# Optimization experiments

Hardware: AMD Instinct MI355X
Metric: run time of the kernel (lower is better)

Reference implementation:

```python
import jax, jax.numpy as jnp
import numpy as np


def setup_inputs() -> dict:
    key = jax.random.key(0)
    B, T, I, H = 64, 512, 1024, 1024
    ks = jax.random.split(key, 9)
    scale_x = 1.0 / np.sqrt(I)
    scale_h = 1.0 / np.sqrt(H)
    inp = {"x": jax.random.normal(ks[0], (B, T, I), jnp.float32)}
    names = [("wxi", "whi"), ("wxf", "whf"), ("wxg", "whg"), ("wxo", "who")]
    for g, (nx, nh) in enumerate(names):
        inp[nx] = jax.random.normal(ks[1 + 2 * g], (I, H), jnp.float32) * scale_x
        inp[nh] = jax.random.normal(ks[2 + 2 * g], (H, H), jnp.float32) * scale_h
    for b in ["bxi", "bhi", "bxf", "bhf", "bxg", "bhg", "bxo", "bho"]:
        inp[b] = jnp.zeros((H,), jnp.float32)
    return inp


def reference(x, wxi, bxi, whi, bhi, wxf, bxf, whf, bhf,
              wxg, bxg, whg, bhg, wxo, bxo, who, bho):
    B, T, I = x.shape
    H = whi.shape[0]
    # Precompute all input projections in one big GEMM: (B,T,4H)
    wx = jnp.concatenate([wxi, wxf, wxg, wxo], axis=1)            # (I,4H)
    bx = jnp.concatenate([bxi + bhi, bxf + bhf, bxg + bhg, bxo + bho])  # fold both biases
    xproj = jnp.einsum('bti,ih->bth', x, wx) + bx                 # (B,T,4H)
    wh = jnp.concatenate([whi, whf, whg, who], axis=1)            # (H,4H)

    def step(carry, xp_t):
        h, c = carry                                              # (B,H) each
        gates = xp_t + h @ wh                                     # (B,4H)
        i, f, g, o = jnp.split(gates, 4, axis=-1)
        i = jax.nn.sigmoid(i)
        f = jax.nn.sigmoid(f)
        g = jnp.tanh(g)
        o = jax.nn.sigmoid(o)
        c = f * c + i * g
        h = o * jnp.tanh(c)
        return (h, c), None

    h0 = jnp.zeros((B, H), x.dtype)
    c0 = jnp.zeros((B, H), x.dtype)
    (h_t, c_t), _ = jax.lax.scan(step, (h0, c0), jnp.swapaxes(xproj, 0, 1))
    return (h_t, c_t)
```

## Files before the change

kernel.cpp:

```cpp
#include <hip/hip_runtime.h>

typedef short bf16x8 __attribute__((ext_vector_type(8)));
typedef float f32x4 __attribute__((ext_vector_type(4)));
typedef unsigned long long u64x2 __attribute__((ext_vector_type(2)));

__device__ __forceinline__ unsigned short f2bf(float f) {
  unsigned u = __float_as_uint(f);
  unsigned r = (u + 0x7FFFu + ((u >> 16) & 1u)) >> 16;
  return (unsigned short)r;
}
__device__ __forceinline__ float bf2f(unsigned short s) {
  return __uint_as_float(((unsigned)s) << 16);
}
__device__ __forceinline__ float sigm(float x) {
  return __builtin_amdgcn_rcpf(1.f + __expf(-x));
}
__device__ __forceinline__ float tanh_a(float x) {
  return 1.f - 2.f * __builtin_amdgcn_rcpf(__expf(2.f * x) + 1.f);
}

__device__ __forceinline__ void gload_lds16(const void* g, void* l) {
  __builtin_amdgcn_global_load_lds(
      (const __attribute__((address_space(1))) unsigned int*)g,
      (__attribute__((address_space(3))) unsigned int*)l, 16, 0, 0);
}

#define ALOAD(p)     __hip_atomic_load((p), __ATOMIC_RELAXED, __HIP_MEMORY_SCOPE_AGENT)
#define ASTORE(p, v) __hip_atomic_store((p), (v), __ATOMIC_RELAXED, __HIP_MEMORY_SCOPE_AGENT)


__global__ void k_cvt_x(const float* __restrict__ x, unsigned short* __restrict__ xb, int n4) {
  int i = blockIdx.x * blockDim.x + threadIdx.x;
  if (i < n4) {
    float4 v = ((const float4*)x)[i];
    ushort4 o;
    o.x = f2bf(v.x); o.y = f2bf(v.y); o.z = f2bf(v.z); o.w = f2bf(v.w);
    ((ushort4*)xb)[i] = o;
  }
}

__global__ void k_pack_w(const float* __restrict__ wxi, const float* __restrict__ wxf,
                         const float* __restrict__ wxg, const float* __restrict__ wxo,
                         const float* __restrict__ whi, const float* __restrict__ whf,
                         const float* __restrict__ whg, const float* __restrict__ who,
                         unsigned short* __restrict__ wxt, unsigned short* __restrict__ whp) {
  const float* srcs[8] = {wxi, wxf, wxg, wxo, whi, whf, whg, who};
  int slab = blockIdx.z;
  const float* src = srcs[slab];
  int gate = slab & 3;
  bool is_wh = slab >= 4;
  __shared__ float tile[32][33];
  int tx = threadIdx.x, ty = threadIdx.y;
  int j0 = blockIdx.x * 32, k0 = blockIdx.y * 32;
  #pragma unroll
  for (int i = 0; i < 32; i += 8)
    tile[ty + i][tx] = src[(size_t)(k0 + ty + i) * 1024 + j0 + tx];
  __syncthreads();
  unsigned short* dst = is_wh ? whp : wxt;
  #pragma unroll
  for (int i = 0; i < 32; i += 8) {
    int j = j0 + ty + i;
    int k = k0 + tx;
    float v = tile[tx][ty + i];
    int row = is_wh ? ((j >> 2) * 16 + gate * 4 + (j & 3)) : (gate * 1024 + j);
    dst[(size_t)row * 1024 + k] = f2bf(v);
  }
}

__global__ void k_bias(const float* bxi, const float* bhi, const float* bxf, const float* bhf,
                       const float* bxg, const float* bhg, const float* bxo, const float* bho,
                       float* __restrict__ bx4) {
  int n = blockIdx.x * 256 + threadIdx.x;
  int gate = n >> 10, j = n & 1023;
  const float* a = gate == 0 ? bxi : gate == 1 ? bxf : gate == 2 ? bxg : bxo;
  const float* b = gate == 0 ? bhi : gate == 1 ? bhf : gate == 2 ? bhg : bho;
  bx4[n] = a[j] + b[j];
}

__global__ void k_init(unsigned short* __restrict__ hbuf, unsigned int* __restrict__ flags) {
  int i = blockIdx.x * 256 + threadIdx.x;
  ASTORE((unsigned long long*)hbuf + i, 0ull);
  if (i < 256) ASTORE(flags + i, 0u);
}


__global__ __launch_bounds__(256) void k_xproj(
    const unsigned short* __restrict__ xb,
    const unsigned short* __restrict__ wxt,
    const float* __restrict__ bx4,
    unsigned short* __restrict__ xp)
{
  __shared__ __align__(16) short As[128 * 64];
  __shared__ __align__(16) short Bs[128 * 64];
  const int tid = threadIdx.x;
  const int bid = blockIdx.x;
  const int m0 = (bid >> 5) * 128;
  const int n0 = (bid & 31) * 128;
  const int lane = tid & 63, w = tid >> 6;
  const int l15 = lane & 15, hi = lane >> 4;
  const int mrow0 = (w >> 1) * 64, ncol0 = (w & 1) * 64;

  f32x4 acc[4][4] = {};
  const char* xbB = (const char*)xb;
  const char* wtB = (const char*)wxt;

  for (int ks = 0; ks < 16; ++ks) {
    #pragma unroll
    for (int c = 0; c < 4; ++c) {
      int d = c * 4096 + tid * 16;
      int r = d >> 7;
      int kb = (d & 127) ^ ((r & 7) << 4);
      gload_lds16(xbB + ((size_t)(m0 + r) * 2048 + ks * 128 + kb), (char*)As + d);
    }
    #pragma unroll
    for (int c = 0; c < 4; ++c) {
      int d = c * 4096 + tid * 16;
      int r = d >> 7;
      int kb = (d & 127) ^ ((r & 7) << 4);
      gload_lds16(wtB + ((size_t)(n0 + r) * 2048 + ks * 128 + kb), (char*)Bs + d);
    }
    __syncthreads();
    #pragma unroll
    for (int kk = 0; kk < 2; ++kk) {
      bf16x8 a[4], b[4];
      #pragma unroll
      for (int mt = 0; mt < 4; ++mt) {
        int r = mrow0 + mt * 16 + l15;
        int byt = r * 128 + ((kk * 64 + hi * 16) ^ ((r & 7) << 4));
        a[mt] = *(const bf16x8*)((const char*)As + byt);
      }
      #pragma unroll
      for (int nt = 0; nt < 4; ++nt) {
        int r = ncol0 + nt * 16 + l15;
        int byt = r * 128 + ((kk * 64 + hi * 16) ^ ((r & 7) << 4));
        b[nt] = *(const bf16x8*)((const char*)Bs + byt);
      }
      #pragma unroll
      for (int mt = 0; mt < 4; ++mt)
        #pragma unroll
        for (int nt = 0; nt < 4; ++nt)
          acc[mt][nt] = __builtin_amdgcn_mfma_f32_16x16x32_bf16(a[mt], b[nt], acc[mt][nt], 0, 0, 0);
    }
    __syncthreads();
  }
  float bias[4];
  int pcol[4];
  #pragma unroll
  for (int nt = 0; nt < 4; ++nt) {
    int n = n0 + ncol0 + nt * 16 + l15;
    bias[nt] = bx4[n];
    int gate = n >> 10, j = n & 1023;
    pcol[nt] = (j >> 2) * 16 + gate * 4 + (j & 3);
  }
  #pragma unroll
  for (int mt = 0; mt < 4; ++mt)
    #pragma unroll
    for (int nt = 0; nt < 4; ++nt) {
      #pragma unroll
      for (int ri = 0; ri < 4; ++ri) {
        int row = m0 + mrow0 + mt * 16 + hi * 4 + ri;
        int prow = (row & 511) * 64 + (row >> 9);
        xp[(size_t)prow * 4096 + pcol[nt]] = f2bf(acc[mt][nt][ri] + bias[nt]);
      }
    }
}


__global__ __launch_bounds__(512, 1) void k_lstm(
    const unsigned short* __restrict__ whp,
    const unsigned short* __restrict__ xp,
    unsigned short* __restrict__ hbuf,
    unsigned int* __restrict__ flags,
    float* __restrict__ out)
{
  const int bid = blockIdx.x;
  const int q = bid >> 5;
  const int cg = bid & 31;
  const int r0 = q * 16;
  const int tid = threadIdx.x;
  const int lane = tid & 63, w = tid >> 6;
  const int l15 = lane & 15, hi = lane >> 4;
  const int gate = l15 >> 2, jj = l15 & 3;

  __shared__ __align__(16) short hs[16 * 1032];

  const unsigned short* wrow = whp + (size_t)((8 * cg + w) * 16 + l15) * 1024 + hi * 8;
  bf16x8 wf[32];
  #pragma unroll
  for (int ks = 0; ks < 32; ++ks) wf[ks] = *(const bf16x8*)(wrow + ks * 32);

  const int hcol = 32 * cg + 4 * w + jj;
  const int pc = (8 * cg + w) * 16 + l15;
  const int base = (lane & 48) | jj;
  const int pbase = lane & 48;
  const int srow = tid >> 5;
  const int scp = tid & 31;
  float cst[4] = {0.f, 0.f, 0.f, 0.f};

  float xpv[4];
  #pragma unroll
  for (int ri = 0; ri < 4; ++ri)
    xpv[ri] = bf2f(xp[(size_t)(r0 + hi * 4 + ri) * 4096 + pc]);

  for (int t = 0; t < 512; ++t) {
    {
      const char* gsrc = (const char*)(hbuf + (t & 1) * 65536 + (r0 + srow) * 1024) + scp * 16;
      u64x2 tmp[4];
      #pragma unroll
      for (int i = 0; i < 4; ++i)
        asm volatile("global_load_dwordx4 %0, %1, off sc0 sc1"
                     : "=v"(tmp[i]) : "v"(gsrc + i * 512) : "memory");
      asm volatile("s_waitcnt vmcnt(0)" ::: "memory");
      __builtin_amdgcn_sched_barrier(0);
      short* ld = hs + srow * 1032 + scp * 8;
      #pragma unroll
      for (int i = 0; i < 4; ++i)
        *(bf16x8*)(ld + i * 256) = __builtin_bit_cast(bf16x8, tmp[i]);
    }
    __syncthreads();

    const short* hsrow = hs + l15 * 1032 + hi * 8;
    f32x4 ac0 = {}, ac1 = {}, ac2 = {}, ac3 = {};
    #pragma unroll
    for (int ks = 0; ks < 32; ks += 4) {
      ac0 = __builtin_amdgcn_mfma_f32_16x16x32_bf16(*(const bf16x8*)(hsrow + ks * 32),       wf[ks],     ac0, 0, 0, 0);
      ac1 = __builtin_amdgcn_mfma_f32_16x16x32_bf16(*(const bf16x8*)(hsrow + (ks + 1) * 32), wf[ks + 1], ac1, 0, 0, 0);
      ac2 = __builtin_amdgcn_mfma_f32_16x16x32_bf16(*(const bf16x8*)(hsrow + (ks + 2) * 32), wf[ks + 2], ac2, 0, 0, 0);
      ac3 = __builtin_amdgcn_mfma_f32_16x16x32_bf16(*(const bf16x8*)(hsrow + (ks + 3) * 32), wf[ks + 3], ac3, 0, 0, 0);
    }
    f32x4 acc = (ac0 + ac1) + (ac2 + ac3);

    float act[4];
    #pragma unroll
    for (int ri = 0; ri < 4; ++ri) {
      float v = acc[ri] + xpv[ri];
      act[ri] = (gate == 2) ? tanh_a(v) : sigm(v);
    }
    float hv[4];
    #pragma unroll
    for (int ri = 0; ri < 4; ++ri) {
      float iv = __shfl(act[ri], base);
      float fv = __shfl(act[ri], base + 4);
      float gv = __shfl(act[ri], base + 8);
      float ov = __shfl(act[ri], base + 12);
      cst[ri] = fv * cst[ri] + iv * gv;
      hv[ri] = ov * tanh_a(cst[ri]);
    }

    if (t == 511) {
      if (gate == 0) {
        #pragma unroll
        for (int ri = 0; ri < 4; ++ri) {
          int b = r0 + hi * 4 + ri;
          out[b * 1024 + hcol] = hv[ri];
          out[65536 + b * 1024 + hcol] = cst[ri];
        }
      }
      break;
    }

    unsigned short* hn = hbuf + ((t + 1) & 1) * 65536;
    #pragma unroll
    for (int ri = 0; ri < 4; ++ri) {
      int hbv = (int)f2bf(hv[ri]);
      int c0 = __shfl(hbv, pbase + 0);
      int c1 = __shfl(hbv, pbase + 1);
      int c2 = __shfl(hbv, pbase + 2);
      int c3 = __shfl(hbv, pbase + 3);
      if (l15 == 0) {
        unsigned lo = ((unsigned)c0 & 0xFFFFu) | ((unsigned)c1 << 16);
        unsigned long long hi64 = ((unsigned)c2 & 0xFFFFu) | ((unsigned)c3 << 16);
        unsigned long long pv = (unsigned long long)lo | (hi64 << 32);
        int row = r0 + hi * 4 + ri;
        ASTORE((unsigned long long*)(hn + row * 1024 + 32 * cg + 4 * w), pv);
      }
    }

    __syncthreads();
    if (tid == 0) ASTORE(flags + bid, (unsigned)(t + 1));

    float nx[4];
    #pragma unroll
    for (int ri = 0; ri < 4; ++ri)
      nx[ri] = bf2f(xp[(size_t)((t + 1) * 64 + r0 + hi * 4 + ri) * 4096 + pc]);

    if (w == 0) {
      const unsigned int* fp = flags + q * 32 + (lane & 31);
      unsigned tgt = (unsigned)(t + 1);
      while (true) {
        unsigned f = ALOAD(fp);
        if (__all(f >= tgt)) break;
        __builtin_amdgcn_s_sleep(1);
      }
    }
    __syncthreads();
    #pragma unroll
    for (int ri = 0; ri < 4; ++ri) xpv[ri] = nx[ri];
  }
}


extern "C" void kernel_launch(void* const* d_in, const int* in_sizes, int n_in,
                              void* d_out, int out_size, void* d_ws, size_t ws_size,
                              hipStream_t stream) {
  const float* x = (const float*)d_in[0];
  const float* wxi = (const float*)d_in[1];
  const float* whi = (const float*)d_in[2];
  const float* wxf = (const float*)d_in[3];
  const float* whf = (const float*)d_in[4];
  const float* wxg = (const float*)d_in[5];
  const float* whg = (const float*)d_in[6];
  const float* wxo = (const float*)d_in[7];
  const float* who = (const float*)d_in[8];

  char* ws = (char*)d_ws;
  unsigned short* xb  = (unsigned short*)(ws);
  unsigned short* wxt = (unsigned short*)(ws + 67108864);
  unsigned short* whp = (unsigned short*)(ws + 75497472);
  unsigned short* xpj = (unsigned short*)(ws + 83886080);
  float*          bx4 = (float*)(ws + 352321536);
  unsigned short* hbuf  = (unsigned short*)(ws + 352337920);
  unsigned int*   flags = (unsigned int*)(ws + 352337920 + 262144);

  k_cvt_x<<<32768, 256, 0, stream>>>(x, xb, 8388608);
  k_pack_w<<<dim3(32, 32, 8), dim3(32, 8), 0, stream>>>(wxi, wxf, wxg, wxo, whi, whf, whg, who, wxt, whp);
  k_bias<<<16, 256, 0, stream>>>((const float*)d_in[9], (const float*)d_in[10],
                                 (const float*)d_in[11], (const float*)d_in[12],
                                 (const float*)d_in[13], (const float*)d_in[14],
                                 (const float*)d_in[15], (const float*)d_in[16], bx4);
  k_init<<<128, 256, 0, stream>>>(hbuf, flags);
  k_xproj<<<8192, 256, 0, stream>>>(xb, wxt, bx4, xpj);

  float* out = (float*)d_out;
  void* args[] = {(void*)&whp, (void*)&xpj, (void*)&hbuf, (void*)&flags, (void*)&out};
  hipLaunchCooperativeKernel((const void*)k_lstm, dim3(128), dim3(512), args, 0, stream);
}
```

Measured before the change: 2.370 ms.

## Fuse step flags into tagged hidden-state words to remove per-step barrier

Each hidden value is published as a 32-bit word carrying the bf16 value plus the producing timestep in the upper bits. Consumers spin directly on the data loads until all tags match, which replaces the separate flag store, spin on flags and extra block barriers. Shared memory for h is double-buffered so only one syncthreads per step remains. This doubles the bytes per h exchange and makes retries load full rows, and it also reuses the x workspace region for the h buffer.

```diff
diff --git a/kernel.cpp b/kernel.cpp
--- a/kernel.cpp
+++ b/kernel.cpp
@@ -2,6 +2,7 @@
 
 typedef short bf16x8 __attribute__((ext_vector_type(8)));
 typedef float f32x4 __attribute__((ext_vector_type(4)));
+typedef unsigned int u32x4 __attribute__((ext_vector_type(4)));
 typedef unsigned long long u64x2 __attribute__((ext_vector_type(2)));
 
 __device__ __forceinline__ unsigned short f2bf(float f) {
@@ -77,10 +78,9 @@
   bx4[n] = a[j] + b[j];
 }
 
-__global__ void k_init(unsigned short* __restrict__ hbuf, unsigned int* __restrict__ flags) {
+__global__ void k_init(unsigned long long* __restrict__ hb) {
   int i = blockIdx.x * 256 + threadIdx.x;
-  ASTORE((unsigned long long*)hbuf + i, 0ull);
-  if (i < 256) ASTORE(flags + i, 0u);
+  ASTORE(hb + i, 0ull);
 }
 
 
@@ -166,11 +166,10 @@
 }
 
 
-__global__ __launch_bounds__(512, 1) void k_lstm(
+__global__ __launch_bounds__(512, 2) void k_lstm(
     const unsigned short* __restrict__ whp,
     const unsigned short* __restrict__ xp,
-    unsigned short* __restrict__ hbuf,
-    unsigned int* __restrict__ flags,
+    unsigned int* __restrict__ hb2,
     float* __restrict__ out)
 {
   const int bid = blockIdx.x;
@@ -182,19 +181,20 @@
   const int l15 = lane & 15, hi = lane >> 4;
   const int gate = l15 >> 2, jj = l15 & 3;
 
-  __shared__ __align__(16) short hs[16 * 1032];
+  __shared__ __align__(16) short hs[2 * 16512];
 
   const unsigned short* wrow = whp + (size_t)((8 * cg + w) * 16 + l15) * 1024 + hi * 8;
   bf16x8 wf[32];
   #pragma unroll
   for (int ks = 0; ks < 32; ++ks) wf[ks] = *(const bf16x8*)(wrow + ks * 32);
-
+  #pragma unroll
+  for (int ks = 0; ks < 32; ++ks) asm volatile("" : "+v"(wf[ks]));
+
+  const int pc = (8 * cg + w) * 16 + l15;
   const int hcol = 32 * cg + 4 * w + jj;
-  const int pc = (8 * cg + w) * 16 + l15;
   const int base = (lane & 48) | jj;
-  const int pbase = lane & 48;
   const int srow = tid >> 5;
-  const int scp = tid & 31;
+  const int scol = (tid & 31) * 32;
   float cst[4] = {0.f, 0.f, 0.f, 0.f};
 
   float xpv[4];
@@ -203,23 +203,44 @@
     xpv[ri] = bf2f(xp[(size_t)(r0 + hi * 4 + ri) * 4096 + pc]);
 
   for (int t = 0; t < 512; ++t) {
-    {
-      const char* gsrc = (const char*)(hbuf + (t & 1) * 65536 + (r0 + srow) * 1024) + scp * 16;
-      u64x2 tmp[4];
-      #pragma unroll
-      for (int i = 0; i < 4; ++i)
-        asm volatile("global_load_dwordx4 %0, %1, off sc0 sc1"
-                     : "=v"(tmp[i]) : "v"(gsrc + i * 512) : "memory");
+    const unsigned int* gsrc = hb2 + (t & 1) * 65536 + (r0 + srow) * 1024 + scol;
+    const unsigned tagpat = (unsigned)t << 16;
+    u32x4 d0, d1, d2, d3, d4, d5, d6, d7;
+    while (true) {
+      asm volatile("global_load_dwordx4 %0, %1, off sc0 sc1" : "=v"(d0) : "v"(gsrc) : "memory");
+      asm volatile("global_load_dwordx4 %0, %1, off sc0 sc1" : "=v"(d1) : "v"(gsrc + 4) : "memory");
+      asm volatile("global_load_dwordx4 %0, %1, off sc0 sc1" : "=v"(d2) : "v"(gsrc + 8) : "memory");
+      asm volatile("global_load_dwordx4 %0, %1, off sc0 sc1" : "=v"(d3) : "v"(gsrc + 12) : "memory");
+      asm volatile("global_load_dwordx4 %0, %1, off sc0 sc1" : "=v"(d4) : "v"(gsrc + 16) : "memory");
+      asm volatile("global_load_dwordx4 %0, %1, off sc0 sc1" : "=v"(d5) : "v"(gsrc + 20) : "memory");
+      asm volatile("global_load_dwordx4 %0, %1, off sc0 sc1" : "=v"(d6) : "v"(gsrc + 24) : "memory");
+      asm volatile("global_load_dwordx4 %0, %1, off sc0 sc1" : "=v"(d7) : "v"(gsrc + 28) : "memory");
       asm volatile("s_waitcnt vmcnt(0)" ::: "memory");
       __builtin_amdgcn_sched_barrier(0);
-      short* ld = hs + srow * 1032 + scp * 8;
-      #pragma unroll
-      for (int i = 0; i < 4; ++i)
-        *(bf16x8*)(ld + i * 256) = __builtin_bit_cast(bf16x8, tmp[i]);
-    }
+      unsigned bad = 0;
+      #define CK(D) bad |= ((D.x ^ tagpat) | (D.y ^ tagpat) | (D.z ^ tagpat) | (D.w ^ tagpat)) & 0xFFFF0000u
+      CK(d0); CK(d1); CK(d2); CK(d3); CK(d4); CK(d5); CK(d6); CK(d7);
+      #undef CK
+      if (__all(bad == 0)) break;
+      __builtin_amdgcn_s_sleep(1);
+    }
+    short* ld = hs + (t & 1) * 16512 + srow * 1032 + scol;
+    u32x4 p0, p1, p2, p3;
+    p0.x = (d0.x & 0xFFFFu) | (d0.y << 16); p0.y = (d0.z & 0xFFFFu) | (d0.w << 16);
+    p0.z = (d1.x & 0xFFFFu) | (d1.y << 16); p0.w = (d1.z & 0xFFFFu) | (d1.w << 16);
+    p1.x = (d2.x & 0xFFFFu) | (d2.y << 16); p1.y = (d2.z & 0xFFFFu) | (d2.w << 16);
+    p1.z = (d3.x & 0xFFFFu) | (d3.y << 16); p1.w = (d3.z & 0xFFFFu) | (d3.w << 16);
+    p2.x = (d4.x & 0xFFFFu) | (d4.y << 16); p2.y = (d4.z & 0xFFFFu) | (d4.w << 16);
+    p2.z = (d5.x & 0xFFFFu) | (d5.y << 16); p2.w = (d5.z & 0xFFFFu) | (d5.w << 16);
+    p3.x = (d6.x & 0xFFFFu) | (d6.y << 16); p3.y = (d6.z & 0xFFFFu) | (d6.w << 16);
+    p3.z = (d7.x & 0xFFFFu) | (d7.y << 16); p3.w = (d7.z & 0xFFFFu) | (d7.w << 16);
+    *(u32x4*)(ld) = p0;
+    *(u32x4*)(ld + 8) = p1;
+    *(u32x4*)(ld + 16) = p2;
+    *(u32x4*)(ld + 24) = p3;
     __syncthreads();
 
-    const short* hsrow = hs + l15 * 1032 + hi * 8;
+    const short* hsrow = hs + (t & 1) * 16512 + l15 * 1032 + hi * 8;
     f32x4 ac0 = {}, ac1 = {}, ac2 = {}, ac3 = {};
     #pragma unroll
     for (int ks = 0; ks < 32; ks += 4) {
@@ -259,41 +280,20 @@
       break;
     }
 
-    unsigned short* hn = hbuf + ((t + 1) & 1) * 65536;
-    #pragma unroll
-    for (int ri = 0; ri < 4; ++ri) {
-      int hbv = (int)f2bf(hv[ri]);
-      int c0 = __shfl(hbv, pbase + 0);
-      int c1 = __shfl(hbv, pbase + 1);
-      int c2 = __shfl(hbv, pbase + 2);
-      int c3 = __shfl(hbv, pbase + 3);
-      if (l15 == 0) {
-        unsigned lo = ((unsigned)c0 & 0xFFFFu) | ((unsigned)c1 << 16);
-        unsigned long long hi64 = ((unsigned)c2 & 0xFFFFu) | ((unsigned)c3 << 16);
-        unsigned long long pv = (unsigned long long)lo | (hi64 << 32);
-        int row = r0 + hi * 4 + ri;
-        ASTORE((unsigned long long*)(hn + row * 1024 + 32 * cg + 4 * w), pv);
-      }
-    }
-
-    __syncthreads();
-    if (tid == 0) ASTORE(flags + bid, (unsigned)(t + 1));
-
     float nx[4];
     #pragma unroll
     for (int ri = 0; ri < 4; ++ri)
       nx[ri] = bf2f(xp[(size_t)((t + 1) * 64 + r0 + hi * 4 + ri) * 4096 + pc]);
 
-    if (w == 0) {
-      const unsigned int* fp = flags + q * 32 + (lane & 31);
-      unsigned tgt = (unsigned)(t + 1);
-      while (true) {
-        unsigned f = ALOAD(fp);
-        if (__all(f >= tgt)) break;
-        __builtin_amdgcn_s_sleep(1);
-      }
-    }
-    __syncthreads();
+    if (gate == 0) {
+      const unsigned ntag = (unsigned)(t + 1) << 16;
+      unsigned int* hb = hb2 + ((t + 1) & 1) * 65536;
+      #pragma unroll
+      for (int ri = 0; ri < 4; ++ri) {
+        int row = r0 + hi * 4 + ri;
+        ASTORE(hb + row * 1024 + hcol, (unsigned)f2bf(hv[ri]) | ntag);
+      }
+    }
     #pragma unroll
     for (int ri = 0; ri < 4; ++ri) xpv[ri] = nx[ri];
   }
@@ -319,8 +319,7 @@
   unsigned short* whp = (unsigned short*)(ws + 75497472);
   unsigned short* xpj = (unsigned short*)(ws + 83886080);
   float*          bx4 = (float*)(ws + 352321536);
-  unsigned short* hbuf  = (unsigned short*)(ws + 352337920);
-  unsigned int*   flags = (unsigned int*)(ws + 352337920 + 262144);
+  unsigned int*   hb2 = (unsigned int*)(ws);
 
   k_cvt_x<<<32768, 256, 0, stream>>>(x, xb, 8388608);
   k_pack_w<<<dim3(32, 32, 8), dim3(32, 8), 0, stream>>>(wxi, wxf, wxg, wxo, whi, whf, whg, who, wxt, whp);
@@ -328,10 +327,10 @@
                                  (const float*)d_in[11], (const float*)d_in[12],
                                  (const float*)d_in[13], (const float*)d_in[14],
                                  (const float*)d_in[15], (const float*)d_in[16], bx4);
-  k_init<<<128, 256, 0, stream>>>(hbuf, flags);
   k_xproj<<<8192, 256, 0, stream>>>(xb, wxt, bx4, xpj);
+  k_init<<<256, 256, 0, stream>>>((unsigned long long*)hb2);
 
   float* out = (float*)d_out;
-  void* args[] = {(void*)&whp, (void*)&xpj, (void*)&hbuf, (void*)&flags, (void*)&out};
+  void* args[] = {(void*)&whp, (void*)&xpj, (void*)&hb2, (void*)&out};
   hipLaunchCooperativeKernel((const void*)k_lstm, dim3(128), dim3(512), args, 0, stream);
 }
```

Result: slower. 3.445 ms (+45.4%).
